# Kernel optimization log

Measured on AMD Instinct MI355X. Metric: run time of the kernel, lower is better.

The kernel has to match this reference:

```python
import jax, jax.numpy as jnp
import numpy as np

jax.config.update("jax_enable_x64", True)

# Module hyperparameters (from init_kwargs)
NUM_EMB = 1_000_000
EMB_DIM = 128
COMPRESSION = 1.0 / 64.0
WEIGHT_SIZE = int(NUM_EMB * EMB_DIM * COMPRESSION)  # 2_000_000 (1D compressed table)

# Hash constants matching the CUDA kernel's multiplicative hash:
# hashed_idx = (index * P1 + dim * P2) mod weight_size
P1 = np.uint64(9824516537)
P2 = np.uint64(57857966300227)

BATCH = 16384
BAG_LEN = 50


def _hashed_idx(indices):
    # indices: [N] int -> hashed positions [N, EMB_DIM] into the 1D weight table
    flat = indices.reshape(-1).astype(jnp.uint64)
    dims = jnp.arange(EMB_DIM, dtype=jnp.uint64)
    h = (flat[:, None] * P1 + dims[None, :] * P2) % jnp.uint64(WEIGHT_SIZE)
    return h.astype(jnp.int64)


def setup_inputs() -> dict:
    key = jax.random.key(0)
    k1, k2 = jax.random.split(key)
    indices = jax.random.randint(k1, (BATCH, BAG_LEN), 0, NUM_EMB, dtype=jnp.int64)
    # reset_parameters(): init.normal_(weight)
    weight = jax.random.normal(k2, (WEIGHT_SIZE,), dtype=jnp.float32)
    return {"weight": weight, "indices": indices}


def reference(weight, indices):
    # 2D indices path: each row is one bag of fixed length; mode='sum'.
    B, L = indices.shape
    hidx = _hashed_idx(indices)                      # [B*L, D]
    emb = weight[hidx].reshape(B, L, EMB_DIM)        # gather from compressed table
    return emb.sum(axis=1)                           # [B, D] per-bag sum
```

## Files before the change

### kernel.cpp

```cpp
#include <hip/hip_runtime.h>
#include <stdint.h>


#define WS       2000000
#define EMB_DIM  128
#define BAG_LEN  50
#define BATCH    16384

#define NBLK     512
#define NBLK_SW  256
#define NTHR     1024
#define BAGS_PB  64
#define SWBAGS   48
#define NPAIR    24
#define SPT      3
#define EXTP     204
#define TILEE    28672
#define NREGS    70
#define SBIG     300227u
#define SENT     0x10000000u

#define OFF_EXT  57344
#define SMEM_SZ  76928

#define GLOAD_LDS16(gp, lp)                                            \
    __builtin_amdgcn_global_load_lds(                                  \
        (const __attribute__((address_space(1))) uint32_t*)(gp),       \
        (__attribute__((address_space(3))) uint32_t*)(lp), 16, 0, 0)

__global__ __launch_bounds__(1024) void conv_bf16(
    const float* __restrict__ w, uint16_t* __restrict__ o)
{
    const int i = (blockIdx.x * 1024 + threadIdx.x) * 4;
    if (i >= WS) return;
    const float4 f = *(const float4*)(w + i);
    uint32_t u0 = __float_as_uint(f.x), u1 = __float_as_uint(f.y);
    uint32_t u2 = __float_as_uint(f.z), u3 = __float_as_uint(f.w);
    ushort4 r;
    r.x = (uint16_t)((u0 + 0x7FFFu + ((u0 >> 16) & 1u)) >> 16);
    r.y = (uint16_t)((u1 + 0x7FFFu + ((u1 >> 16) & 1u)) >> 16);
    r.z = (uint16_t)((u2 + 0x7FFFu + ((u2 >> 16) & 1u)) >> 16);
    r.w = (uint16_t)((u3 + 0x7FFFu + ((u3 >> 16) & 1u)) >> 16);
    *(ushort4*)(o + i) = r;
}

__global__ __launch_bounds__(NTHR, 8) void heb_bf16(
    const uint16_t* __restrict__ wbf,
    const int*      __restrict__ indices,
    float*          __restrict__ out)
{
    __shared__ __align__(16) uint8_t smem[SMEM_SZ];
    const int tid = threadIdx.x;

    if (blockIdx.x >= NBLK_SW) {
        const int gi   = blockIdx.x - NBLK_SW;
        const int bagL = tid >> 6;
        const int d0   = tid & 63;
        uint32_t* ag = (uint32_t*)smem;

        for (int p = tid; p < 16 * BAG_LEN; p += NTHR) {
            int b = p / 50, i = p - b * 50;
            uint64_t idx = (uint64_t)(uint32_t)
                indices[(gi * BAGS_PB + SWBAGS + b) * BAG_LEN + i];
            ag[p] = (uint32_t)((idx * 9824516537ull) % (uint64_t)WS);
        }
        __syncthreads();

        const uint32_t c0 = ((uint32_t)d0 * SBIG) % (uint32_t)WS;
        const uint32_t c1 = ((uint32_t)(d0 + 64) * SBIG) % (uint32_t)WS;
        const uint32_t* agb = ag + bagL * BAG_LEN;
        float a0 = 0.0f, a1 = 0.0f;
#pragma unroll 10
        for (int i = 0; i < BAG_LEN; ++i) {
            const uint32_t a = agb[i];
            uint32_t u0 = a + c0; u0 = (u0 >= (uint32_t)WS) ? u0 - WS : u0;
            uint32_t u1 = a + c1; u1 = (u1 >= (uint32_t)WS) ? u1 - WS : u1;
            const uint32_t r0 = (uint32_t)wbf[u0];
            const uint32_t r1 = (uint32_t)wbf[u1];
            a0 += __uint_as_float(r0 << 16);
            a1 += __uint_as_float(r1 << 16);
        }
        const size_t ob =
            (size_t)(gi * BAGS_PB + SWBAGS + bagL) * EMB_DIM;
        out[ob + d0]      = a0;
        out[ob + d0 + 64] = a1;
        return;
    }

    const int d       = tid & 127;
    const int g       = tid >> 7;
    const int bagBase = blockIdx.x * BAGS_PB;

    uint16_t* tile0 = (uint16_t*)&smem[0];
    uint32_t* ext   = (uint32_t*)&smem[OFF_EXT];
    uint32_t* araw  = (uint32_t*)&smem[0];
    uint32_t* S     = (uint32_t*)&smem[9984];

    for (int p = tid; p < NPAIR * EXTP; p += NTHR) ext[p] = SENT;
    for (int p = tid; p < SWBAGS * BAG_LEN; p += NTHR) {
        uint32_t b = (uint32_t)p / 50u;
        uint32_t i = (uint32_t)p - b * 50u;
        uint64_t idx = (uint64_t)(uint32_t)
            indices[bagBase * BAG_LEN + p];
        araw[b * 52 + i] = (uint32_t)((idx * 9824516537ull) % (uint64_t)WS);
    }
    __syncthreads();

    for (int p = tid; p < SWBAGS * BAG_LEN; p += NTHR) {
        uint32_t b = (uint32_t)p / 50u;
        uint32_t i = (uint32_t)p - b * 50u;
        uint32_t v = araw[b * 52 + i];
        int rank = 0;
        for (int q = 0; q < BAG_LEN; ++q) {
            uint32_t w = araw[b * 52 + q];
            rank += (w < v || (w == v && q < (int)i)) ? 1 : 0;
        }
        S[b * 52 + rank] = v;
    }
    __syncthreads();

    for (int p = tid; p < SWBAGS * BAG_LEN; p += NTHR) {
        uint32_t bag = (uint32_t)p / 50u;
        uint32_t i   = (uint32_t)p - bag * 50u;
        uint32_t pr  = bag >> 1, b = bag & 1u;
        uint32_t v = S[bag * 52 + i];
        const uint32_t* T = &S[(bag ^ 1u) * 52];
        uint32_t key = b ? v + 1u : v;
        int lo = 0, hi = 50;
        while (lo < hi) {
            int mid = (lo + hi) >> 1;
            bool lt = T[mid] < key;
            lo = lt ? mid + 1 : lo;
            hi = lt ? hi : mid;
        }
        uint32_t* eo = ext + pr * EXTP;
        int rk = (int)i + lo;
        eo[rk]       = (v << 1) | b;
        eo[rk + 100] = ((v + (uint32_t)WS) << 1) | b;
    }
    __syncthreads();

    const uint32_t c  = ((uint32_t)d * SBIG) % (uint32_t)WS;
    const uint32_t C2 = (uint32_t)(((int)c - WS) * 2);
    const uint32_t limit2 = ((uint32_t)WS - c) << 1;

    uint32_t kq4[SPT], K4[SPT];
    float    s0r[SPT], s1r[SPT];
#pragma unroll
    for (int qi = 0; qi < SPT; ++qi) {
        const uint32_t rbase = (uint32_t)(g * SPT + qi) * EXTP;
        int lo = 0, hi = 100;
        while (lo < hi) {
            int mid = (lo + hi) >> 1;
            bool lt = ext[rbase + (uint32_t)mid] < limit2;
            lo = lt ? mid + 1 : lo;
            hi = lt ? hi : mid;
        }
        kq4[qi] = rbase + (uint32_t)lo;
        K4[qi]  = ext[rbase + (uint32_t)lo];
        s0r[qi] = 0.0f; s1r[qi] = 0.0f;
    }

    for (int r = 0; r < NREGS; ++r) {
        const int rlo = r * TILEE;
        const int len = (TILEE < WS - rlo) ? TILEE : (WS - rlo);

        __syncthreads();
        for (int s = tid; s < (len >> 3); s += NTHR)
            GLOAD_LDS16(wbf + rlo + (s << 3), tile0 + (s << 3));
        __syncthreads();

        const uint32_t CLr = C2 - ((uint32_t)rlo << 1);
        const uint32_t LIM = (uint32_t)len << 1;

#pragma unroll
        for (int qi = 0; qi < SPT; ++qi) {
            uint32_t kq = kq4[qi], K = K4[qi];
            float s0 = s0r[qi], s1 = s1r[qi];
            uint32_t u = K + CLr;
            while (u < LIM) {
                const uint32_t raw =
                    *(const uint16_t*)(smem + (u & ~1u));
                K = ext[kq + 1u];
                ++kq;
                const float v = __uint_as_float(raw << 16);
                const bool odd = (u & 1u) != 0u;
                s0 += odd ? 0.0f : v;
                s1 += odd ? v : 0.0f;
                u = K + CLr;
            }
            kq4[qi] = kq; K4[qi] = K;
            s0r[qi] = s0; s1r[qi] = s1;
        }
    }

#pragma unroll
    for (int qi = 0; qi < SPT; ++qi) {
        const int bag = g * 6 + (qi << 1);
        out[(size_t)(bagBase + bag) * EMB_DIM + d]     = s0r[qi];
        out[(size_t)(bagBase + bag + 1) * EMB_DIM + d] = s1r[qi];
    }
}

#define RSIZE_FB 32768
#define NREG_FB  62
#define EXT_N    104
#define SENT4    0x10000000u

__global__ __launch_bounds__(NTHR, 4) void heb_single(
    const float* __restrict__ weight,
    const int*   __restrict__ indices,
    float*       __restrict__ out)
{
    __shared__ __align__(16) float tile[RSIZE_FB];
    __shared__ uint32_t ext4[BAGS_PB][EXT_N];
    const int tid = threadIdx.x, d = tid & 127, bag_lo = tid >> 7;
    const int bagBase = blockIdx.x * BAGS_PB;
    uint32_t* araw = (uint32_t*)&tile[0];
    for (int p = tid; p < BAGS_PB * BAG_LEN; p += NTHR) {
        uint32_t g = (uint32_t)p / 50u, i = (uint32_t)p - g * 50u;
        uint64_t idx = (uint64_t)(uint32_t)indices[bagBase * BAG_LEN + p];
        araw[g * 52 + i] = (uint32_t)((idx * 9824516537ull) % (uint64_t)WS);
    }
    __syncthreads();
    for (int p = tid; p < BAGS_PB * BAG_LEN; p += NTHR) {
        uint32_t g = (uint32_t)p / 50u, i = (uint32_t)p - g * 50u;
        uint32_t v = araw[g * 52 + i];
        int rank = 0;
        for (int q = 0; q < BAG_LEN; ++q) {
            uint32_t w = araw[g * 52 + q];
            rank += (w < v || (w == v && q < (int)i)) ? 1 : 0;
        }
        ext4[g][rank] = v << 2;
        ext4[g][rank + 50] = (v + (uint32_t)WS) << 2;
    }
    for (int p = tid; p < BAGS_PB * 4; p += NTHR)
        ext4[p >> 2][100 + (p & 3)] = SENT4;
    __syncthreads();
    const uint32_t c = ((uint32_t)d * SBIG) % (uint32_t)WS;
    const uint32_t C4 = (uint32_t)(((int)c - WS) * 4);
    const uint32_t wmc4 = ((uint32_t)WS - c) << 2;
    uint32_t t4[8], h4[8]; float sm[8];
#pragma unroll
    for (int k = 0; k < 8; ++k) {
        const uint32_t* eg = &ext4[(bag_lo << 3) + k][0];
        int nlow = 0;
        for (int q = 0; q < BAG_LEN; ++q) nlow += (eg[q] < wmc4) ? 1 : 0;
        t4[k] = (uint32_t)nlow << 2; h4[k] = eg[nlow] + C4; sm[k] = 0.0f;
    }
    for (int r = 0; r < NREG_FB; ++r) {
        const int lo = r * RSIZE_FB;
        const int len = (RSIZE_FB < WS - lo) ? RSIZE_FB : (WS - lo);
        __syncthreads();
        for (int s = tid; s < (len >> 2); s += NTHR)
            GLOAD_LDS16(weight + lo + (s << 2), &tile[s << 2]);
        __syncthreads();
        const uint32_t lo4 = ((uint32_t)lo) << 2;
        const uint32_t hi4 = (r == NREG_FB - 1) ? (uint32_t)(4 * WS)
                                                : lo4 + ((uint32_t)RSIZE_FB << 2);
        const char* tb = (const char*)&tile[0];
#pragma unroll
        for (int k = 0; k < 8; ++k) {
            const char* eg = (const char*)&ext4[(bag_lo << 3) + k][0];
            uint32_t t_ = t4[k], h_ = h4[k]; float s_ = sm[k];
            while (h_ < hi4) {
                s_ += *(const float*)(tb + (h_ - lo4));
                t_ += 4u;
                h_ = *(const uint32_t*)(eg + t_) + C4;
            }
            t4[k] = t_; h4[k] = h_; sm[k] = s_;
        }
    }
#pragma unroll
    for (int k = 0; k < 8; ++k)
        out[(size_t)(bagBase + (bag_lo << 3) + k) * EMB_DIM + d] = sm[k];
}

extern "C" void kernel_launch(void* const* d_in, const int* in_sizes, int n_in,
                              void* d_out, int out_size, void* d_ws, size_t ws_size,
                              hipStream_t stream)
{
    const float* weight  = (const float*)d_in[0];
    const int*   indices = (const int*)d_in[1];
    float*       out     = (float*)d_out;

    if (ws_size >= (size_t)WS * sizeof(uint16_t)) {
        uint16_t* wbf = (uint16_t*)d_ws;
        conv_bf16<<<(WS / 4 + 1023) / 1024, 1024, 0, stream>>>(weight, wbf);
        heb_bf16<<<NBLK, NTHR, 0, stream>>>(wbf, indices, out);
    } else {
        heb_single<<<NBLK, NTHR, 0, stream>>>(weight, indices, out);
    }
}
```

Measured before the change: 254.3 us.

## Drop hybrid direct-gather blocks; run sweep path on all blocks with 32 bags each

Result: faster. 211.3 us, median of 2 (-16.9%).

```diff
diff --git a/kernel.cpp b/kernel.cpp
--- a/kernel.cpp
+++ b/kernel.cpp
@@ -8,20 +8,18 @@
 #define BATCH    16384
 
 #define NBLK     512
-#define NBLK_SW  256
 #define NTHR     1024
-#define BAGS_PB  64
-#define SWBAGS   48
-#define NPAIR    24
-#define SPT      3
+#define BPB      32
+#define NPAIR    16
+#define SPT      2
 #define EXTP     204
-#define TILEE    28672
-#define NREGS    70
+#define TILEE    32768
+#define NREGS    62
 #define SBIG     300227u
 #define SENT     0x10000000u
 
-#define OFF_EXT  57344
-#define SMEM_SZ  76928
+#define OFF_EXT  65536
+#define SMEM_SZ  78592
 
 #define GLOAD_LDS16(gp, lp)                                            \
     __builtin_amdgcn_global_load_lds(                                  \
@@ -50,54 +48,19 @@
     float*          __restrict__ out)
 {
     __shared__ __align__(16) uint8_t smem[SMEM_SZ];
-    const int tid = threadIdx.x;
-
-    if (blockIdx.x >= NBLK_SW) {
-        const int gi   = blockIdx.x - NBLK_SW;
-        const int bagL = tid >> 6;
-        const int d0   = tid & 63;
-        uint32_t* ag = (uint32_t*)smem;
-
-        for (int p = tid; p < 16 * BAG_LEN; p += NTHR) {
-            int b = p / 50, i = p - b * 50;
-            uint64_t idx = (uint64_t)(uint32_t)
-                indices[(gi * BAGS_PB + SWBAGS + b) * BAG_LEN + i];
-            ag[p] = (uint32_t)((idx * 9824516537ull) % (uint64_t)WS);
-        }
-        __syncthreads();
-
-        const uint32_t c0 = ((uint32_t)d0 * SBIG) % (uint32_t)WS;
-        const uint32_t c1 = ((uint32_t)(d0 + 64) * SBIG) % (uint32_t)WS;
-        const uint32_t* agb = ag + bagL * BAG_LEN;
-        float a0 = 0.0f, a1 = 0.0f;
-#pragma unroll 10
-        for (int i = 0; i < BAG_LEN; ++i) {
-            const uint32_t a = agb[i];
-            uint32_t u0 = a + c0; u0 = (u0 >= (uint32_t)WS) ? u0 - WS : u0;
-            uint32_t u1 = a + c1; u1 = (u1 >= (uint32_t)WS) ? u1 - WS : u1;
-            const uint32_t r0 = (uint32_t)wbf[u0];
-            const uint32_t r1 = (uint32_t)wbf[u1];
-            a0 += __uint_as_float(r0 << 16);
-            a1 += __uint_as_float(r1 << 16);
-        }
-        const size_t ob =
-            (size_t)(gi * BAGS_PB + SWBAGS + bagL) * EMB_DIM;
-        out[ob + d0]      = a0;
-        out[ob + d0 + 64] = a1;
-        return;
-    }
-
+
+    const int tid     = threadIdx.x;
     const int d       = tid & 127;
     const int g       = tid >> 7;
-    const int bagBase = blockIdx.x * BAGS_PB;
+    const int bagBase = blockIdx.x * BPB;
 
     uint16_t* tile0 = (uint16_t*)&smem[0];
     uint32_t* ext   = (uint32_t*)&smem[OFF_EXT];
     uint32_t* araw  = (uint32_t*)&smem[0];
-    uint32_t* S     = (uint32_t*)&smem[9984];
+    uint32_t* S     = (uint32_t*)&smem[6656];
 
     for (int p = tid; p < NPAIR * EXTP; p += NTHR) ext[p] = SENT;
-    for (int p = tid; p < SWBAGS * BAG_LEN; p += NTHR) {
+    for (int p = tid; p < BPB * BAG_LEN; p += NTHR) {
         uint32_t b = (uint32_t)p / 50u;
         uint32_t i = (uint32_t)p - b * 50u;
         uint64_t idx = (uint64_t)(uint32_t)
@@ -106,7 +69,7 @@
     }
     __syncthreads();
 
-    for (int p = tid; p < SWBAGS * BAG_LEN; p += NTHR) {
+    for (int p = tid; p < BPB * BAG_LEN; p += NTHR) {
         uint32_t b = (uint32_t)p / 50u;
         uint32_t i = (uint32_t)p - b * 50u;
         uint32_t v = araw[b * 52 + i];
@@ -119,7 +82,7 @@
     }
     __syncthreads();
 
-    for (int p = tid; p < SWBAGS * BAG_LEN; p += NTHR) {
+    for (int p = tid; p < BPB * BAG_LEN; p += NTHR) {
         uint32_t bag = (uint32_t)p / 50u;
         uint32_t i   = (uint32_t)p - bag * 50u;
         uint32_t pr  = bag >> 1, b = bag & 1u;
@@ -196,12 +159,13 @@
 
 #pragma unroll
     for (int qi = 0; qi < SPT; ++qi) {
-        const int bag = g * 6 + (qi << 1);
+        const int bag = (g << 2) + (qi << 1);
         out[(size_t)(bagBase + bag) * EMB_DIM + d]     = s0r[qi];
         out[(size_t)(bagBase + bag + 1) * EMB_DIM + d] = s1r[qi];
     }
 }
 
+#define BAGS_FB  64
 #define RSIZE_FB 32768
 #define NREG_FB  62
 #define EXT_N    104
@@ -213,17 +177,17 @@
     float*       __restrict__ out)
 {
     __shared__ __align__(16) float tile[RSIZE_FB];
-    __shared__ uint32_t ext4[BAGS_PB][EXT_N];
+    __shared__ uint32_t ext4[BAGS_FB][EXT_N];
     const int tid = threadIdx.x, d = tid & 127, bag_lo = tid >> 7;
-    const int bagBase = blockIdx.x * BAGS_PB;
+    const int bagBase = blockIdx.x * BAGS_FB;
     uint32_t* araw = (uint32_t*)&tile[0];
-    for (int p = tid; p < BAGS_PB * BAG_LEN; p += NTHR) {
+    for (int p = tid; p < BAGS_FB * BAG_LEN; p += NTHR) {
         uint32_t g = (uint32_t)p / 50u, i = (uint32_t)p - g * 50u;
         uint64_t idx = (uint64_t)(uint32_t)indices[bagBase * BAG_LEN + p];
         araw[g * 52 + i] = (uint32_t)((idx * 9824516537ull) % (uint64_t)WS);
     }
     __syncthreads();
-    for (int p = tid; p < BAGS_PB * BAG_LEN; p += NTHR) {
+    for (int p = tid; p < BAGS_FB * BAG_LEN; p += NTHR) {
         uint32_t g = (uint32_t)p / 50u, i = (uint32_t)p - g * 50u;
         uint32_t v = araw[g * 52 + i];
         int rank = 0;
@@ -234,7 +198,7 @@
         ext4[g][rank] = v << 2;
         ext4[g][rank + 50] = (v + (uint32_t)WS) << 2;
     }
-    for (int p = tid; p < BAGS_PB * 4; p += NTHR)
+    for (int p = tid; p < BAGS_FB * 4; p += NTHR)
         ext4[p >> 2][100 + (p & 3)] = SENT4;
     __syncthreads();
     const uint32_t c = ((uint32_t)d * SBIG) % (uint32_t)WS;
@@ -289,6 +253,6 @@
         conv_bf16<<<(WS / 4 + 1023) / 1024, 1024, 0, stream>>>(weight, wbf);
         heb_bf16<<<NBLK, NTHR, 0, stream>>>(wbf, indices, out);
     } else {
-        heb_single<<<NBLK, NTHR, 0, stream>>>(weight, indices, out);
-    }
-}
+        heb_single<<<256, NTHR, 0, stream>>>(weight, indices, out);
+    }
+}
```
